# Kernel tuning notes

Hardware: AMD Instinct MI355X
Metric: run time of the kernel (lower is better)

Reference implementation:

```python
import jax, jax.numpy as jnp
import numpy as np

B, Q, H, V = 32, 180, 768, 19004


def setup_inputs() -> dict:
    key = jax.random.key(0)
    k1, k2, k3, k4 = jax.random.split(key, 4)
    output_tokens = jax.random.normal(k1, (B, Q, H), dtype=jnp.float32)
    W_embed = jax.random.normal(k2, (V, H), dtype=jnp.float32) * 0.02
    b_embed = jax.random.normal(k3, (V,), dtype=jnp.float32) * 0.02
    parcel_ids = jax.random.randint(k4, (V,), 0, Q, dtype=jnp.int32)
    return {"output_tokens": output_tokens, "W_embed": W_embed,
            "b_embed": b_embed, "parcel_ids": parcel_ids}


def reference(output_tokens, W_embed, b_embed, parcel_ids):
    # embed: Linear(hidden_dim -> num_hemi_voxels): [B, Q, V]
    pred = jnp.einsum('bqh,vh->bqv', output_tokens, W_embed) + b_embed
    # movedim(1, -1): [B, V, Q]
    pred = jnp.moveaxis(pred, 1, -1)
    # parcel_mask: one-hot [V, Q] (each voxel assigned to exactly one parcel)
    num_q = output_tokens.shape[1]
    mask = jax.nn.one_hot(parcel_ids, num_q, dtype=pred.dtype)  # [V, Q]
    # multiply by mask and sum over parcel/query axis -> [B, V]
    return jnp.sum(pred * mask, axis=-1)
```

## Files before the change

kernel.cpp:

```cpp
#include <hip/hip_runtime.h>
#include <hip/hip_bf16.h>

#define BB 32
#define QQ 180
#define HH 768
#define VV 19004
#define VB 64
#define KH 384
#define SB 19008
#define MAXDESC 480
#define STRIDE 392
#define NB 80
#define CH 238

#define WS_H      0
#define WS_NTOT   65536
#define WS_DESC   66560
#define WS_SORTED 74752
#define WS_POSOF  151552
#define WS_RES    229376

typedef __attribute__((ext_vector_type(8))) short short8v;
typedef __attribute__((ext_vector_type(4))) float f32x4;

__device__ __forceinline__ unsigned pk2(float lo, float hi) {
    __hip_bfloat162 r = __float22bfloat162_rn(make_float2(lo, hi));
    unsigned u;
    __builtin_memcpy(&u, &r, 4);
    return u;
}

__global__ void hist_k(const int* __restrict__ pid, int* __restrict__ h) {
    __shared__ int lc[QQ];
    const int t = threadIdx.x, b = blockIdx.x;
    if (t < QQ) lc[t] = 0;
    __syncthreads();
    const int v = b * CH + t;
    if (t < CH && v < VV) atomicAdd(&lc[pid[v]], 1);
    __syncthreads();
    if (t < QQ) h[b * QQ + t] = lc[t];
}

__global__ void scat_k(const int* __restrict__ pid, const int* __restrict__ h,
                       int* __restrict__ sorted, int* __restrict__ posOf,
                       int4* __restrict__ desc, int* __restrict__ ntot) {
    __shared__ int s1[256];
    __shared__ int s2[256];
    __shared__ int cur[QQ];
    const int t = threadIdx.x, b = blockIdx.x;
    int c = 0, mybase = 0;
    if (t < QQ) {
        for (int i = 0; i < NB; ++i) {
            if (i == b) mybase = c;
            c += h[i * QQ + t];
        }
    }
    s1[t] = c;
    __syncthreads();
    for (int off = 1; off < 256; off <<= 1) {
        int a = (t >= off) ? s1[t - off] : 0;
        __syncthreads();
        s1[t] += a;
        __syncthreads();
    }
    const int qs = s1[t] - c;
    if (t < QQ) cur[t] = qs + mybase;
    if (b == 0) {
        const int nch = (c + VB - 1) / VB;
        s2[t] = nch;
        __syncthreads();
        for (int off = 1; off < 256; off <<= 1) {
            int a = (t >= off) ? s2[t - off] : 0;
            __syncthreads();
            s2[t] += a;
            __syncthreads();
        }
        if (t < QQ) {
            const int cb = s2[t] - nch;
            for (int j = 0; j < nch; ++j)
                desc[cb + j] = make_int4(t, qs + j * VB, min(VB, c - j * VB), 0);
        }
        if (t == 255) *ntot = s2[255];
    }
    __syncthreads();
    const int v = b * CH + t;
    if (t < CH && v < VV) {
        const int q = pid[v];
        const int pos = atomicAdd(&cur[q], 1);
        sorted[pos] = v;
        posOf[v] = pos;
    }
}

__launch_bounds__(256)
__global__ void main_k(const float* __restrict__ OT, const float* __restrict__ W,
                       const int* __restrict__ sorted, const int4* __restrict__ desc,
                       const int* __restrict__ ntot, float* __restrict__ res) {
    const int nt = *ntot;
    const int bid = blockIdx.x;
    const int ci = bid >> 1;
    if (ci >= nt) return;
    const int kh = bid & 1;
    const int4 d = desc[ci];
    const int q     = __builtin_amdgcn_readfirstlane(d.x);
    const int start = __builtin_amdgcn_readfirstlane(d.y);
    const int len   = __builtin_amdgcn_readfirstlane(d.z);
    const int tid = threadIdx.x;

    __shared__ short OTlds[BB * STRIDE];

    {
        const int r = tid >> 3;
        const int o = tid & 7;
        const float* src = OT + ((size_t)r * QQ + q) * HH + kh * KH + o * 8;
        short* dst = &OTlds[r * STRIDE + o * 8];
#pragma unroll
        for (int it = 0; it < 6; ++it) {
            const float4 f0 = *(const float4*)(src + it * 64);
            const float4 f1 = *(const float4*)(src + it * 64 + 4);
            int4 p;
            p.x = (int)pk2(f0.x, f0.y); p.y = (int)pk2(f0.z, f0.w);
            p.z = (int)pk2(f1.x, f1.y); p.w = (int)pk2(f1.z, f1.w);
            *(int4*)(dst + it * 64) = p;
        }
    }

    const int lane = tid & 63;
    const int w = tid >> 6;
    const int co = lane & 15;
    const int kq = lane >> 4;
    const int vl = 16 * w + co;
    const int vg = sorted[start + min(vl, len - 1)];
    const float4* wp4 = (const float4*)(W + (size_t)vg * HH + kh * KH + kq * 8);
    const short* a0 = &OTlds[co * STRIDE + kq * 8];

    float4 wf[24];
#pragma unroll
    for (int kk = 0; kk < 12; ++kk) {
        wf[2 * kk]     = wp4[kk * 8];
        wf[2 * kk + 1] = wp4[kk * 8 + 1];
    }

    __syncthreads();

    f32x4 acc0 = {0.f, 0.f, 0.f, 0.f};
    f32x4 acc1 = {0.f, 0.f, 0.f, 0.f};
#pragma unroll
    for (int kk = 0; kk < 12; ++kk) {
        const float4 wf0 = wf[2 * kk];
        const float4 wf1 = wf[2 * kk + 1];
        int4 p;
        p.x = (int)pk2(wf0.x, wf0.y); p.y = (int)pk2(wf0.z, wf0.w);
        p.z = (int)pk2(wf1.x, wf1.y); p.w = (int)pk2(wf1.z, wf1.w);
        short8v bf;
        __builtin_memcpy(&bf, &p, 16);
        const short8v a0v = *(const short8v*)(a0 + kk * 32);
        const short8v a1v = *(const short8v*)(a0 + 16 * STRIDE + kk * 32);
        acc0 = __builtin_amdgcn_mfma_f32_16x16x32_bf16(a0v, bf, acc0, 0, 0, 0);
        acc1 = __builtin_amdgcn_mfma_f32_16x16x32_bf16(a1v, bf, acc1, 0, 0, 0);
    }

    if (vl < len) {
        float* rp = res + (size_t)(kh * BB) * SB + start + vl;
#pragma unroll
        for (int r2 = 0; r2 < 4; ++r2) {
            rp[(size_t)(kq * 4 + r2) * SB]      = acc0[r2];
            rp[(size_t)(16 + kq * 4 + r2) * SB] = acc1[r2];
        }
    }
}

__global__ void combine_k(const float* __restrict__ res, const int* __restrict__ posOf,
                          const float* __restrict__ bias, float* __restrict__ out) {
    const int v = blockIdx.x * 256 + threadIdx.x;
    if (v >= VV) return;
    const int b = blockIdx.y;
    const int pos = posOf[v];
    const float s = res[(size_t)b * SB + pos] + res[(size_t)(BB + b) * SB + pos];
    out[(size_t)b * VV + v] = s + bias[v];
}

extern "C" void kernel_launch(void* const* d_in, const int* in_sizes, int n_in,
                              void* d_out, int out_size, void* d_ws, size_t ws_size,
                              hipStream_t stream) {
    const float* OT   = (const float*)d_in[0];
    const float* W    = (const float*)d_in[1];
    const float* bias = (const float*)d_in[2];
    const int*   pid  = (const int*)d_in[3];
    float* out = (float*)d_out;

    char* ws = (char*)d_ws;
    int*   h      = (int*)(ws + WS_H);
    int*   ntot   = (int*)(ws + WS_NTOT);
    int4*  desc   = (int4*)(ws + WS_DESC);
    int*   sorted = (int*)(ws + WS_SORTED);
    int*   posOf  = (int*)(ws + WS_POSOF);
    float* res    = (float*)(ws + WS_RES);

    hist_k<<<NB, 256, 0, stream>>>(pid, h);
    scat_k<<<NB, 256, 0, stream>>>(pid, h, sorted, posOf, desc, ntot);

    main_k<<<2 * MAXDESC, 256, 0, stream>>>(OT, W, sorted, desc, ntot, res);

    combine_k<<<dim3((VV + 255) / 256, BB), 256, 0, stream>>>(res, posOf, bias, out);
}
```

Measured before the change: 41.67 us.

## Drop split-K halves in main kernel and pipeline W loads across full H

The main kernel no longer splits the hidden dimension into two halves across blocks. Each block now covers all 768 hidden elements, loading twice the OT tile into LDS and software-pipelining the W register loads in three batches interleaved with the MFMA steps. The combine kernel reads a single partial result instead of summing two, and half as many blocks are launched. This removes the duplicated OT staging and the extra partial-result traffic, at the cost of fewer blocks for parallelism, more LDS per block and more registers.

```diff
diff --git a/kernel.cpp b/kernel.cpp
--- a/kernel.cpp
+++ b/kernel.cpp
@@ -6,10 +6,9 @@
 #define HH 768
 #define VV 19004
 #define VB 64
-#define KH 384
 #define SB 19008
 #define MAXDESC 480
-#define STRIDE 392
+#define ST 776
 #define NB 80
 #define CH 238
 
@@ -92,30 +91,41 @@
     }
 }
 
+#define MSTEP(kk, F0, F1)                                                     \
+    {                                                                         \
+        int4 p_;                                                              \
+        p_.x = (int)pk2((F0).x, (F0).y); p_.y = (int)pk2((F0).z, (F0).w);     \
+        p_.z = (int)pk2((F1).x, (F1).y); p_.w = (int)pk2((F1).z, (F1).w);     \
+        short8v bf_;                                                          \
+        __builtin_memcpy(&bf_, &p_, 16);                                      \
+        const short8v a0v_ = *(const short8v*)(a0p + (kk) * 32);              \
+        const short8v a1v_ = *(const short8v*)(a0p + 16 * ST + (kk) * 32);    \
+        acc0 = __builtin_amdgcn_mfma_f32_16x16x32_bf16(a0v_, bf_, acc0, 0, 0, 0); \
+        acc1 = __builtin_amdgcn_mfma_f32_16x16x32_bf16(a1v_, bf_, acc1, 0, 0, 0); \
+    }
+
 __launch_bounds__(256)
 __global__ void main_k(const float* __restrict__ OT, const float* __restrict__ W,
                        const int* __restrict__ sorted, const int4* __restrict__ desc,
                        const int* __restrict__ ntot, float* __restrict__ res) {
     const int nt = *ntot;
-    const int bid = blockIdx.x;
-    const int ci = bid >> 1;
+    const int ci = blockIdx.x;
     if (ci >= nt) return;
-    const int kh = bid & 1;
     const int4 d = desc[ci];
     const int q     = __builtin_amdgcn_readfirstlane(d.x);
     const int start = __builtin_amdgcn_readfirstlane(d.y);
     const int len   = __builtin_amdgcn_readfirstlane(d.z);
     const int tid = threadIdx.x;
 
-    __shared__ short OTlds[BB * STRIDE];
+    __shared__ short OTlds[BB * ST];
 
     {
         const int r = tid >> 3;
         const int o = tid & 7;
-        const float* src = OT + ((size_t)r * QQ + q) * HH + kh * KH + o * 8;
-        short* dst = &OTlds[r * STRIDE + o * 8];
-#pragma unroll
-        for (int it = 0; it < 6; ++it) {
+        const float* src = OT + ((size_t)r * QQ + q) * HH + o * 8;
+        short* dst = &OTlds[r * ST + o * 8];
+#pragma unroll
+        for (int it = 0; it < 12; ++it) {
             const float4 f0 = *(const float4*)(src + it * 64);
             const float4 f1 = *(const float4*)(src + it * 64 + 4);
             int4 p;
@@ -131,37 +141,45 @@
     const int kq = lane >> 4;
     const int vl = 16 * w + co;
     const int vg = sorted[start + min(vl, len - 1)];
-    const float4* wp4 = (const float4*)(W + (size_t)vg * HH + kh * KH + kq * 8);
-    const short* a0 = &OTlds[co * STRIDE + kq * 8];
-
-    float4 wf[24];
+    const float4* wp4 = (const float4*)(W + (size_t)vg * HH + kq * 8);
+    const short* a0p = &OTlds[co * ST + kq * 8];
+
+    float4 wa[24];
 #pragma unroll
     for (int kk = 0; kk < 12; ++kk) {
-        wf[2 * kk]     = wp4[kk * 8];
-        wf[2 * kk + 1] = wp4[kk * 8 + 1];
+        wa[2 * kk]     = wp4[kk * 8];
+        wa[2 * kk + 1] = wp4[kk * 8 + 1];
     }
 
     __syncthreads();
 
     f32x4 acc0 = {0.f, 0.f, 0.f, 0.f};
     f32x4 acc1 = {0.f, 0.f, 0.f, 0.f};
-#pragma unroll
-    for (int kk = 0; kk < 12; ++kk) {
-        const float4 wf0 = wf[2 * kk];
-        const float4 wf1 = wf[2 * kk + 1];
-        int4 p;
-        p.x = (int)pk2(wf0.x, wf0.y); p.y = (int)pk2(wf0.z, wf0.w);
-        p.z = (int)pk2(wf1.x, wf1.y); p.w = (int)pk2(wf1.z, wf1.w);
-        short8v bf;
-        __builtin_memcpy(&bf, &p, 16);
-        const short8v a0v = *(const short8v*)(a0 + kk * 32);
-        const short8v a1v = *(const short8v*)(a0 + 16 * STRIDE + kk * 32);
-        acc0 = __builtin_amdgcn_mfma_f32_16x16x32_bf16(a0v, bf, acc0, 0, 0, 0);
-        acc1 = __builtin_amdgcn_mfma_f32_16x16x32_bf16(a1v, bf, acc1, 0, 0, 0);
-    }
+    float4 wb0[12], wb1[12];
+
+#pragma unroll
+    for (int kk = 0; kk < 6; ++kk) MSTEP(kk, wa[2 * kk], wa[2 * kk + 1]);
+#pragma unroll
+    for (int j = 0; j < 6; ++j) {
+        wb0[2 * j]     = wp4[(12 + j) * 8];
+        wb0[2 * j + 1] = wp4[(12 + j) * 8 + 1];
+    }
+#pragma unroll
+    for (int kk = 6; kk < 12; ++kk) MSTEP(kk, wa[2 * kk], wa[2 * kk + 1]);
+#pragma unroll
+    for (int j = 0; j < 6; ++j) {
+        wb1[2 * j]     = wp4[(18 + j) * 8];
+        wb1[2 * j + 1] = wp4[(18 + j) * 8 + 1];
+    }
+#pragma unroll
+    for (int kk = 12; kk < 18; ++kk)
+        MSTEP(kk, wb0[2 * (kk - 12)], wb0[2 * (kk - 12) + 1]);
+#pragma unroll
+    for (int kk = 18; kk < 24; ++kk)
+        MSTEP(kk, wb1[2 * (kk - 18)], wb1[2 * (kk - 18) + 1]);
 
     if (vl < len) {
-        float* rp = res + (size_t)(kh * BB) * SB + start + vl;
+        float* rp = res + start + vl;
 #pragma unroll
         for (int r2 = 0; r2 < 4; ++r2) {
             rp[(size_t)(kq * 4 + r2) * SB]      = acc0[r2];
@@ -176,8 +194,7 @@
     if (v >= VV) return;
     const int b = blockIdx.y;
     const int pos = posOf[v];
-    const float s = res[(size_t)b * SB + pos] + res[(size_t)(BB + b) * SB + pos];
-    out[(size_t)b * VV + v] = s + bias[v];
+    out[(size_t)b * VV + v] = res[(size_t)b * SB + pos] + bias[v];
 }
 
 extern "C" void kernel_launch(void* const* d_in, const int* in_sizes, int n_in,
@@ -200,7 +217,7 @@
     hist_k<<<NB, 256, 0, stream>>>(pid, h);
     scat_k<<<NB, 256, 0, stream>>>(pid, h, sorted, posOf, desc, ntot);
 
-    main_k<<<2 * MAXDESC, 256, 0, stream>>>(OT, W, sorted, desc, ntot, res);
+    main_k<<<MAXDESC, 256, 0, stream>>>(OT, W, sorted, desc, ntot, res);
 
     combine_k<<<dim3((VV + 255) / 256, BB), 256, 0, stream>>>(res, posOf, bias, out);
 }
```

After: 40.85 us. -2.0%, faster.
